# Kernel optimization log

Hardware: AMD Instinct MI355X
Metric: run time of the kernel (lower is better)

## Reference

```python
import jax, jax.numpy as jnp
import numpy as np

U, I, D = 50000, 25000, 128          # users, items, emb_size
E = 1_000_000                        # user-item interactions
L = 3                                # num_layers
B = 4096                             # BPR batch size
N = U + I                            # total graph nodes


def setup_inputs() -> dict:
    key = jax.random.key(0)
    k1, k2, k3, k4, k5, k6, k7 = jax.random.split(key, 7)
    # Xavier-ish embedding tables
    user_emb = jax.random.normal(k1, (U, D), jnp.float32) * 0.1
    item_emb = jax.random.normal(k2, (I, D), jnp.float32) * 0.1
    # random bipartite interactions -> symmetric COO adjacency over N nodes
    eu = jax.random.randint(k3, (E,), 0, U)            # user node ids
    ei = jax.random.randint(k4, (E,), 0, I) + U        # item node ids (offset)
    adj_row = jnp.concatenate([eu, ei]).astype(jnp.int32)   # [2E]
    adj_col = jnp.concatenate([ei, eu]).astype(jnp.int32)   # [2E]
    # symmetric normalization D^-1/2 A D^-1/2 (matches create_adj_mat)
    deg = jax.ops.segment_sum(jnp.ones(2 * E, jnp.float32), adj_row, num_segments=N)
    d_inv = jnp.where(deg > 0, deg ** -0.5, 0.0)
    adj_vals = d_inv[adj_row] * d_inv[adj_col]               # [2E] float32
    users = jax.random.randint(k5, (B,), 0, U).astype(jnp.int32)
    pos_items = jax.random.randint(k6, (B,), 0, I).astype(jnp.int32)
    neg_items = jax.random.randint(k7, (B,), 0, I).astype(jnp.int32)
    return dict(user_emb=user_emb, item_emb=item_emb, adj_row=adj_row,
                adj_col=adj_col, adj_vals=adj_vals, users=users,
                pos_items=pos_items, neg_items=neg_items)


def _spmm(vals, row, col, x):
    # sparse [N,N] @ dense [N,D] via gather + segment_sum
    return jax.ops.segment_sum(vals[:, None] * x[col], row, num_segments=N)


def reference(user_emb, item_emb, adj_row, adj_col, adj_vals,
              users, pos_items, neg_items):
    ego = jnp.concatenate([user_emb, item_emb], axis=0)      # [N, D]
    # FAITHFUL to the torch source: ego_embeddings is never reassigned inside
    # the layer loop, so every one of the L layer outputs equals A @ ego.
    # mean(stack([ego, A@ego, ..., A@ego])) == (ego + L * A@ego) / (L + 1)
    h = _spmm(adj_vals, adj_row, adj_col, ego)               # [N, D]
    final = (ego + L * h) / (L + 1)                          # mean over L+1 layers
    u_final = final[:U]
    i_final = final[U:]
    u_g = u_final[users]                                     # [B, D]
    pos_i_g = i_final[pos_items]                             # [B, D]
    neg_i_g = i_final[neg_items]                             # [B, D]
    return (u_g, pos_i_g, neg_i_g, i_final)
```

## Files before the change

### kernel.cpp

```cpp
#include <hip/hip_runtime.h>
#include <hip/hip_bf16.h>

#define U_CNT 50000
#define I_CNT 25000
#define D_DIM 128
#define E_CNT 1000000
#define B_CNT 4096
#define ICAP 96
#define UCAP 64
#define PNCAP 16
#define BM_WORDS 1600
#define IRANGE (I_CNT / 8)
#define URANGE (U_CNT / 8)
#define NGROUP 1000
#define CHUNK  (E_CNT / NGROUP)
#define BUCKET_BLKS (NGROUP * 8)
#define CVT_BLKS 3125
#define GI_BLKS (8 * 782)
#define GU_BLKS (B_CNT / 4)

typedef int    vi4 __attribute__((ext_vector_type(4)));
typedef float  vf4 __attribute__((ext_vector_type(4)));
typedef float  vf2 __attribute__((ext_vector_type(2)));
typedef unsigned vu4 __attribute__((ext_vector_type(4)));


__device__ __forceinline__ unsigned pack_bf2(float lo, float hi) {
    __hip_bfloat16 a = __float2bfloat16(lo);
    __hip_bfloat16 b = __float2bfloat16(hi);
    unsigned short ua = *reinterpret_cast<unsigned short*>(&a);
    unsigned short ub = *reinterpret_cast<unsigned short*>(&b);
    return ((unsigned)ub << 16) | ua;
}
__device__ __forceinline__ float bf_lo(unsigned w) { return __uint_as_float(w << 16); }
__device__ __forceinline__ float bf_hi(unsigned w) { return __uint_as_float(w & 0xffff0000u); }

__global__ __launch_bounds__(256) void prep_kernel(
        const int* __restrict__ users,
        const int* __restrict__ pos_items,
        const int* __restrict__ neg_items,
        unsigned*  __restrict__ bitmap,
        int*       __restrict__ slot,
        int*       __restrict__ pncnt,
        int*       __restrict__ pnbuck) {
    const int i = blockIdx.x * blockDim.x + threadIdx.x;
    if (i < B_CNT) {
        const int u = users[i];
        atomicOr(&bitmap[u >> 5], 1u << (u & 31));
        atomicCAS(&slot[u], 0, i + 1);
    }
    if (i < 2 * B_CNT) {
        const int idx = (i < B_CNT) ? pos_items[i] : neg_items[i - B_CNT];
        const int c = atomicAdd(&pncnt[idx], 1);
        if (c < PNCAP) pnbuck[idx * PNCAP + c] = B_CNT + i;
    }
}

__global__ __launch_bounds__(256) void bucket_cvt_kernel(
        const int*      __restrict__ adj_row,
        const int*      __restrict__ adj_col,
        const float*    __restrict__ adj_vals,
        const float*    __restrict__ user_emb,
        const unsigned* __restrict__ bitmap,
        const int*      __restrict__ slot,
        int*  __restrict__ icnt,  int*  __restrict__ ucnt,
        int2* __restrict__ ibuck, int2* __restrict__ ubuck,
        unsigned* __restrict__ ue16) {
    if (blockIdx.x < BUCKET_BLKS) {
        const unsigned x = blockIdx.x & 7;
        const int      g = blockIdx.x >> 3;
        const int base = g * CHUNK + (int)threadIdx.x * 4;
        if (base >= g * CHUNK + CHUNK) return;

        const vi4 uu = __builtin_nontemporal_load((const vi4*)(adj_row  + base));
        const vi4 tt = __builtin_nontemporal_load((const vi4*)(adj_col  + base));
        const vf4 vv = __builtin_nontemporal_load((const vf4*)(adj_vals + base));
        const unsigned us[4] = {(unsigned)uu.x, (unsigned)uu.y,
                                (unsigned)uu.z, (unsigned)uu.w};
        const unsigned ts[4] = {(unsigned)(tt.x - U_CNT), (unsigned)(tt.y - U_CNT),
                                (unsigned)(tt.z - U_CNT), (unsigned)(tt.w - U_CNT)};
        const float    vs[4] = {vv.x, vv.y, vv.z, vv.w};
#pragma unroll
        for (int k = 0; k < 4; ++k) {
            const unsigned u = us[k], t = ts[k];
            const int vb = __float_as_int(vs[k]);
            if (t / IRANGE == x) {
                const int c = atomicAdd(&icnt[t], 1);
                ibuck[(size_t)t * ICAP + c] = make_int2((int)u, vb);
            }
            if (u / URANGE == x) {
                if ((bitmap[u >> 5] >> (u & 31)) & 1u) {
                    const int j0 = slot[u] - 1;
                    const int c2 = atomicAdd(&ucnt[j0], 1);
                    ubuck[(size_t)j0 * UCAP + c2] = make_int2((int)t, vb);
                }
            }
        }
    } else {
        const int bid = blockIdx.x - BUCKET_BLKS;
        int i = bid * 1024 + threadIdx.x;
#pragma unroll
        for (int r = 0; r < 4; ++r, i += 256) {
            const vf2 f = __builtin_nontemporal_load(((const vf2*)user_emb) + i);
            __builtin_nontemporal_store(pack_bf2(f.x, f.y), ue16 + i);
        }
    }
}

__global__ __launch_bounds__(256) void gather_kernel(
        const float*    __restrict__ user_emb,
        const float*    __restrict__ item_emb,
        const unsigned* __restrict__ ue16,
        const int*      __restrict__ users,
        const int*      __restrict__ slot,
        const int*      __restrict__ icnt,
        const int*      __restrict__ ucnt,
        const int*      __restrict__ pncnt,
        const int*      __restrict__ pnbuck,
        const int2*     __restrict__ ibuck,
        const int2*     __restrict__ ubuck,
        float*          __restrict__ out) {
    const int lane = threadIdx.x & 63;
    const int wib  = threadIdx.x >> 6;

    if (blockIdx.x < GI_BLKS) {
        const int x  = blockIdx.x & 7;
        const int g  = blockIdx.x >> 3;
        const int li = g * 4 + wib;
        if (li >= IRANGE) return;
        const int t = x * IRANGE + li;

        const int n   = min(icnt[t], ICAP);
        const int2* b = ibuck + (size_t)t * ICAP;
        const int sub = lane >> 4;
        const int cl  = lane & 15;
        float a0=0.f,a1=0.f,a2=0.f,a3=0.f,a4=0.f,a5=0.f,a6=0.f,a7=0.f;

        int q = 0;
        for (; q + 8 <= n; q += 8) {
            const int2 eA = b[q + sub];
            const int2 eB = b[q + 4 + sub];
            const vu4 wA = *(const vu4*)(ue16 + (size_t)eA.x * 64 + cl * 4);
            const vu4 wB = *(const vu4*)(ue16 + (size_t)eB.x * 64 + cl * 4);
            const float vA = __int_as_float(eA.y), vB = __int_as_float(eB.y);
            a0 += vA*bf_lo(wA.x) + vB*bf_lo(wB.x);
            a1 += vA*bf_hi(wA.x) + vB*bf_hi(wB.x);
            a2 += vA*bf_lo(wA.y) + vB*bf_lo(wB.y);
            a3 += vA*bf_hi(wA.y) + vB*bf_hi(wB.y);
            a4 += vA*bf_lo(wA.z) + vB*bf_lo(wB.z);
            a5 += vA*bf_hi(wA.z) + vB*bf_hi(wB.z);
            a6 += vA*bf_lo(wA.w) + vB*bf_lo(wB.w);
            a7 += vA*bf_hi(wA.w) + vB*bf_hi(wB.w);
        }
        if (q + 4 <= n) {
            const int2 e = b[q + sub];
            const vu4 wv = *(const vu4*)(ue16 + (size_t)e.x * 64 + cl * 4);
            const float v = __int_as_float(e.y);
            a0 += v*bf_lo(wv.x); a1 += v*bf_hi(wv.x);
            a2 += v*bf_lo(wv.y); a3 += v*bf_hi(wv.y);
            a4 += v*bf_lo(wv.z); a5 += v*bf_hi(wv.z);
            a6 += v*bf_lo(wv.w); a7 += v*bf_hi(wv.w);
            q += 4;
        }
        if (q < n) {
            const int r = q + sub;
            if (r < n) {
                const int2 e = b[r];
                const vu4 wv = *(const vu4*)(ue16 + (size_t)e.x * 64 + cl * 4);
                const float v = __int_as_float(e.y);
                a0 += v*bf_lo(wv.x); a1 += v*bf_hi(wv.x);
                a2 += v*bf_lo(wv.y); a3 += v*bf_hi(wv.y);
                a4 += v*bf_lo(wv.z); a5 += v*bf_hi(wv.z);
                a6 += v*bf_lo(wv.w); a7 += v*bf_hi(wv.w);
            }
        }
        a0 += __shfl_xor(a0, 16); a0 += __shfl_xor(a0, 32);
        a1 += __shfl_xor(a1, 16); a1 += __shfl_xor(a1, 32);
        a2 += __shfl_xor(a2, 16); a2 += __shfl_xor(a2, 32);
        a3 += __shfl_xor(a3, 16); a3 += __shfl_xor(a3, 32);
        a4 += __shfl_xor(a4, 16); a4 += __shfl_xor(a4, 32);
        a5 += __shfl_xor(a5, 16); a5 += __shfl_xor(a5, 32);
        a6 += __shfl_xor(a6, 16); a6 += __shfl_xor(a6, 32);
        a7 += __shfl_xor(a7, 16); a7 += __shfl_xor(a7, 32);

        if (sub == 0) {
            const float* ie = item_emb + (size_t)t * D_DIM + cl * 8;
            const vf4 g0 = __builtin_nontemporal_load((const vf4*)ie);
            const vf4 g1 = __builtin_nontemporal_load((const vf4*)(ie + 4));
            vf4 o0, o1;
            o0.x = (g0.x + 3.0f*a0)*0.25f; o0.y = (g0.y + 3.0f*a1)*0.25f;
            o0.z = (g0.z + 3.0f*a2)*0.25f; o0.w = (g0.w + 3.0f*a3)*0.25f;
            o1.x = (g1.x + 3.0f*a4)*0.25f; o1.y = (g1.y + 3.0f*a5)*0.25f;
            o1.z = (g1.z + 3.0f*a6)*0.25f; o1.w = (g1.w + 3.0f*a7)*0.25f;
            float* orow = out + (size_t)(3 * B_CNT + t) * D_DIM + cl * 8;
            __builtin_nontemporal_store(o0, (vf4*)orow);
            __builtin_nontemporal_store(o1, (vf4*)(orow + 4));
            const int pn = min(pncnt[t], PNCAP);
            for (int c = 0; c < pn; ++c) {
                const int row = pnbuck[t * PNCAP + c];
                float* pr = out + (size_t)row * D_DIM + cl * 8;
                __builtin_nontemporal_store(o0, (vf4*)pr);
                __builtin_nontemporal_store(o1, (vf4*)(pr + 4));
            }
        }
    } else {
        const int j = (blockIdx.x - GI_BLKS) * 4 + wib;
        const int u  = users[j];
        const int j0 = slot[u] - 1;
        const int n  = min(ucnt[j0], UCAP);
        const int2* b = ubuck + (size_t)j0 * UCAP;
        float ax = 0.0f, ay = 0.0f;
        int q = 0;
        for (; q + 4 <= n; q += 4) {
            const int2 e0 = b[q], e1 = b[q+1], e2 = b[q+2], e3 = b[q+3];
            const float2 x0 = ((const float2*)(item_emb + (size_t)e0.x * D_DIM))[lane];
            const float2 x1 = ((const float2*)(item_emb + (size_t)e1.x * D_DIM))[lane];
            const float2 x2 = ((const float2*)(item_emb + (size_t)e2.x * D_DIM))[lane];
            const float2 x3 = ((const float2*)(item_emb + (size_t)e3.x * D_DIM))[lane];
            const float v0 = __int_as_float(e0.y), v1 = __int_as_float(e1.y);
            const float v2 = __int_as_float(e2.y), v3 = __int_as_float(e3.y);
            ax += v0*x0.x + v1*x1.x + v2*x2.x + v3*x3.x;
            ay += v0*x0.y + v1*x1.y + v2*x2.y + v3*x3.y;
        }
        for (; q < n; ++q) {
            const int2 e = b[q];
            const float2 xx = ((const float2*)(item_emb + (size_t)e.x * D_DIM))[lane];
            const float v = __int_as_float(e.y);
            ax += v * xx.x;
            ay += v * xx.y;
        }
        const float2 eg = ((const float2*)(user_emb + (size_t)u * D_DIM))[lane];
        float2 o;
        o.x = (eg.x + 3.0f * ax) * 0.25f;
        o.y = (eg.y + 3.0f * ay) * 0.25f;
        ((float2*)(out + (size_t)j * D_DIM))[lane] = o;
    }
}

extern "C" void kernel_launch(void* const* d_in, const int* in_sizes, int n_in,
                              void* d_out, int out_size, void* d_ws, size_t ws_size,
                              hipStream_t stream) {
    const float* user_emb  = (const float*)d_in[0];
    const float* item_emb  = (const float*)d_in[1];
    const int*   adj_row   = (const int*)  d_in[2];
    const int*   adj_col   = (const int*)  d_in[3];
    const float* adj_vals  = (const float*)d_in[4];
    const int*   users     = (const int*)  d_in[5];
    const int*   pos_items = (const int*)  d_in[6];
    const int*   neg_items = (const int*)  d_in[7];
    float* out = (float*)d_out;

    unsigned* bitmap = (unsigned*)d_ws;
    int* slot  = (int*)(bitmap + BM_WORDS);
    int* icnt  = slot + U_CNT;
    int* ucnt  = icnt + I_CNT;
    int* pncnt = ucnt + B_CNT;
    int2* ibuck = (int2*)(pncnt + I_CNT);
    int2* ubuck = ibuck + (size_t)I_CNT * ICAP;
    int*  pnbuck = (int*)(ubuck + (size_t)B_CNT * UCAP);
    unsigned* ue16 = (unsigned*)(pnbuck + (size_t)I_CNT * PNCAP);

    const size_t zero_ints = BM_WORDS + U_CNT + I_CNT + B_CNT + I_CNT;
    hipMemsetAsync(bitmap, 0, zero_ints * sizeof(int), stream);

    prep_kernel<<<(2 * B_CNT + 255) / 256, 256, 0, stream>>>(
        users, pos_items, neg_items, bitmap, slot, pncnt, pnbuck);

    bucket_cvt_kernel<<<BUCKET_BLKS + CVT_BLKS, 256, 0, stream>>>(
        adj_row, adj_col, adj_vals, user_emb, bitmap, slot,
        icnt, ucnt, ibuck, ubuck, ue16);

    gather_kernel<<<GI_BLKS + GU_BLKS, 256, 0, stream>>>(
        user_emb, item_emb, ue16, users, slot, icnt, ucnt,
        pncnt, pnbuck, ibuck, ubuck, out);
}
```

Measured before the change: 206.1 us.

## Pack adjacency bucket records into 32 bits and drop slot zeroing

```diff
diff --git a/kernel.cpp b/kernel.cpp
--- a/kernel.cpp
+++ b/kernel.cpp
@@ -1,5 +1,6 @@
 #include <hip/hip_runtime.h>
 #include <hip/hip_bf16.h>
+#include <hip/hip_fp16.h>
 
 #define U_CNT 50000
 #define I_CNT 25000
@@ -19,9 +20,9 @@
 #define GI_BLKS (8 * 782)
 #define GU_BLKS (B_CNT / 4)
 
-typedef int    vi4 __attribute__((ext_vector_type(4)));
-typedef float  vf4 __attribute__((ext_vector_type(4)));
-typedef float  vf2 __attribute__((ext_vector_type(2)));
+typedef int      vi4 __attribute__((ext_vector_type(4)));
+typedef float    vf4 __attribute__((ext_vector_type(4)));
+typedef float    vf2 __attribute__((ext_vector_type(2)));
 typedef unsigned vu4 __attribute__((ext_vector_type(4)));
 
 
@@ -35,19 +36,27 @@
 __device__ __forceinline__ float bf_lo(unsigned w) { return __uint_as_float(w << 16); }
 __device__ __forceinline__ float bf_hi(unsigned w) { return __uint_as_float(w & 0xffff0000u); }
 
+__device__ __forceinline__ unsigned pack_rec(unsigned id, float v) {
+    const __half h = __float2half(v);
+    return id | ((unsigned)__half_as_ushort(h) << 16);
+}
+__device__ __forceinline__ float rec_val(unsigned rec) {
+    return __half2float(__ushort_as_half((unsigned short)(rec >> 16)));
+}
+
 __global__ __launch_bounds__(256) void prep_kernel(
         const int* __restrict__ users,
         const int* __restrict__ pos_items,
         const int* __restrict__ neg_items,
         unsigned*  __restrict__ bitmap,
-        int*       __restrict__ slot,
+        int*       __restrict__ flag,
         int*       __restrict__ pncnt,
         int*       __restrict__ pnbuck) {
     const int i = blockIdx.x * blockDim.x + threadIdx.x;
     if (i < B_CNT) {
         const int u = users[i];
         atomicOr(&bitmap[u >> 5], 1u << (u & 31));
-        atomicCAS(&slot[u], 0, i + 1);
+        flag[u] = i;
     }
     if (i < 2 * B_CNT) {
         const int idx = (i < B_CNT) ? pos_items[i] : neg_items[i - B_CNT];
@@ -62,9 +71,9 @@
         const float*    __restrict__ adj_vals,
         const float*    __restrict__ user_emb,
         const unsigned* __restrict__ bitmap,
-        const int*      __restrict__ slot,
-        int*  __restrict__ icnt,  int*  __restrict__ ucnt,
-        int2* __restrict__ ibuck, int2* __restrict__ ubuck,
+        const int*      __restrict__ flag,
+        int*      __restrict__ icnt,  int*      __restrict__ ucnt,
+        unsigned* __restrict__ ibuck, unsigned* __restrict__ ubuck,
         unsigned* __restrict__ ue16) {
     if (blockIdx.x < BUCKET_BLKS) {
         const unsigned x = blockIdx.x & 7;
@@ -83,16 +92,15 @@
 #pragma unroll
         for (int k = 0; k < 4; ++k) {
             const unsigned u = us[k], t = ts[k];
-            const int vb = __float_as_int(vs[k]);
             if (t / IRANGE == x) {
                 const int c = atomicAdd(&icnt[t], 1);
-                ibuck[(size_t)t * ICAP + c] = make_int2((int)u, vb);
+                ibuck[(size_t)t * ICAP + c] = pack_rec(u, vs[k]);
             }
             if (u / URANGE == x) {
                 if ((bitmap[u >> 5] >> (u & 31)) & 1u) {
-                    const int j0 = slot[u] - 1;
+                    const int j0 = flag[u];
                     const int c2 = atomicAdd(&ucnt[j0], 1);
-                    ubuck[(size_t)j0 * UCAP + c2] = make_int2((int)t, vb);
+                    ubuck[(size_t)j0 * UCAP + c2] = pack_rec(t, vs[k]);
                 }
             }
         }
@@ -112,13 +120,13 @@
         const float*    __restrict__ item_emb,
         const unsigned* __restrict__ ue16,
         const int*      __restrict__ users,
-        const int*      __restrict__ slot,
+        const int*      __restrict__ flag,
         const int*      __restrict__ icnt,
         const int*      __restrict__ ucnt,
         const int*      __restrict__ pncnt,
         const int*      __restrict__ pnbuck,
-        const int2*     __restrict__ ibuck,
-        const int2*     __restrict__ ubuck,
+        const unsigned* __restrict__ ibuck,
+        const unsigned* __restrict__ ubuck,
         float*          __restrict__ out) {
     const int lane = threadIdx.x & 63;
     const int wib  = threadIdx.x >> 6;
@@ -130,19 +138,19 @@
         if (li >= IRANGE) return;
         const int t = x * IRANGE + li;
 
-        const int n   = min(icnt[t], ICAP);
-        const int2* b = ibuck + (size_t)t * ICAP;
+        const int n = min(icnt[t], ICAP);
+        const unsigned* b = ibuck + (size_t)t * ICAP;
         const int sub = lane >> 4;
         const int cl  = lane & 15;
         float a0=0.f,a1=0.f,a2=0.f,a3=0.f,a4=0.f,a5=0.f,a6=0.f,a7=0.f;
 
         int q = 0;
         for (; q + 8 <= n; q += 8) {
-            const int2 eA = b[q + sub];
-            const int2 eB = b[q + 4 + sub];
-            const vu4 wA = *(const vu4*)(ue16 + (size_t)eA.x * 64 + cl * 4);
-            const vu4 wB = *(const vu4*)(ue16 + (size_t)eB.x * 64 + cl * 4);
-            const float vA = __int_as_float(eA.y), vB = __int_as_float(eB.y);
+            const unsigned eA = b[q + sub];
+            const unsigned eB = b[q + 4 + sub];
+            const vu4 wA = *(const vu4*)(ue16 + (size_t)(eA & 0xFFFFu) * 64 + cl * 4);
+            const vu4 wB = *(const vu4*)(ue16 + (size_t)(eB & 0xFFFFu) * 64 + cl * 4);
+            const float vA = rec_val(eA), vB = rec_val(eB);
             a0 += vA*bf_lo(wA.x) + vB*bf_lo(wB.x);
             a1 += vA*bf_hi(wA.x) + vB*bf_hi(wB.x);
             a2 += vA*bf_lo(wA.y) + vB*bf_lo(wB.y);
@@ -153,9 +161,9 @@
             a7 += vA*bf_hi(wA.w) + vB*bf_hi(wB.w);
         }
         if (q + 4 <= n) {
-            const int2 e = b[q + sub];
-            const vu4 wv = *(const vu4*)(ue16 + (size_t)e.x * 64 + cl * 4);
-            const float v = __int_as_float(e.y);
+            const unsigned e = b[q + sub];
+            const vu4 wv = *(const vu4*)(ue16 + (size_t)(e & 0xFFFFu) * 64 + cl * 4);
+            const float v = rec_val(e);
             a0 += v*bf_lo(wv.x); a1 += v*bf_hi(wv.x);
             a2 += v*bf_lo(wv.y); a3 += v*bf_hi(wv.y);
             a4 += v*bf_lo(wv.z); a5 += v*bf_hi(wv.z);
@@ -165,9 +173,9 @@
         if (q < n) {
             const int r = q + sub;
             if (r < n) {
-                const int2 e = b[r];
-                const vu4 wv = *(const vu4*)(ue16 + (size_t)e.x * 64 + cl * 4);
-                const float v = __int_as_float(e.y);
+                const unsigned e = b[r];
+                const vu4 wv = *(const vu4*)(ue16 + (size_t)(e & 0xFFFFu) * 64 + cl * 4);
+                const float v = rec_val(e);
                 a0 += v*bf_lo(wv.x); a1 += v*bf_hi(wv.x);
                 a2 += v*bf_lo(wv.y); a3 += v*bf_hi(wv.y);
                 a4 += v*bf_lo(wv.z); a5 += v*bf_hi(wv.z);
@@ -206,26 +214,26 @@
     } else {
         const int j = (blockIdx.x - GI_BLKS) * 4 + wib;
         const int u  = users[j];
-        const int j0 = slot[u] - 1;
+        const int j0 = flag[u];
         const int n  = min(ucnt[j0], UCAP);
-        const int2* b = ubuck + (size_t)j0 * UCAP;
+        const unsigned* b = ubuck + (size_t)j0 * UCAP;
         float ax = 0.0f, ay = 0.0f;
         int q = 0;
         for (; q + 4 <= n; q += 4) {
-            const int2 e0 = b[q], e1 = b[q+1], e2 = b[q+2], e3 = b[q+3];
-            const float2 x0 = ((const float2*)(item_emb + (size_t)e0.x * D_DIM))[lane];
-            const float2 x1 = ((const float2*)(item_emb + (size_t)e1.x * D_DIM))[lane];
-            const float2 x2 = ((const float2*)(item_emb + (size_t)e2.x * D_DIM))[lane];
-            const float2 x3 = ((const float2*)(item_emb + (size_t)e3.x * D_DIM))[lane];
-            const float v0 = __int_as_float(e0.y), v1 = __int_as_float(e1.y);
-            const float v2 = __int_as_float(e2.y), v3 = __int_as_float(e3.y);
+            const unsigned e0 = b[q], e1 = b[q+1], e2 = b[q+2], e3 = b[q+3];
+            const float2 x0 = ((const float2*)(item_emb + (size_t)(e0 & 0xFFFFu) * D_DIM))[lane];
+            const float2 x1 = ((const float2*)(item_emb + (size_t)(e1 & 0xFFFFu) * D_DIM))[lane];
+            const float2 x2 = ((const float2*)(item_emb + (size_t)(e2 & 0xFFFFu) * D_DIM))[lane];
+            const float2 x3 = ((const float2*)(item_emb + (size_t)(e3 & 0xFFFFu) * D_DIM))[lane];
+            const float v0 = rec_val(e0), v1 = rec_val(e1);
+            const float v2 = rec_val(e2), v3 = rec_val(e3);
             ax += v0*x0.x + v1*x1.x + v2*x2.x + v3*x3.x;
             ay += v0*x0.y + v1*x1.y + v2*x2.y + v3*x3.y;
         }
         for (; q < n; ++q) {
-            const int2 e = b[q];
-            const float2 xx = ((const float2*)(item_emb + (size_t)e.x * D_DIM))[lane];
-            const float v = __int_as_float(e.y);
+            const unsigned e = b[q];
+            const float2 xx = ((const float2*)(item_emb + (size_t)(e & 0xFFFFu) * D_DIM))[lane];
+            const float v = rec_val(e);
             ax += v * xx.x;
             ay += v * xx.y;
         }
@@ -251,26 +259,26 @@
     float* out = (float*)d_out;
 
     unsigned* bitmap = (unsigned*)d_ws;
-    int* slot  = (int*)(bitmap + BM_WORDS);
-    int* icnt  = slot + U_CNT;
+    int* icnt  = (int*)(bitmap + BM_WORDS);
     int* ucnt  = icnt + I_CNT;
     int* pncnt = ucnt + B_CNT;
-    int2* ibuck = (int2*)(pncnt + I_CNT);
-    int2* ubuck = ibuck + (size_t)I_CNT * ICAP;
-    int*  pnbuck = (int*)(ubuck + (size_t)B_CNT * UCAP);
-    unsigned* ue16 = (unsigned*)(pnbuck + (size_t)I_CNT * PNCAP);
-
-    const size_t zero_ints = BM_WORDS + U_CNT + I_CNT + B_CNT + I_CNT;
+    int* flag  = pncnt + I_CNT;
+    int* pnbuck = flag + U_CNT;
+    unsigned* ibuck = (unsigned*)(pnbuck + (size_t)I_CNT * PNCAP);
+    unsigned* ubuck = ibuck + (size_t)I_CNT * ICAP;
+    unsigned* ue16  = ubuck + (size_t)B_CNT * UCAP;
+
+    const size_t zero_ints = BM_WORDS + I_CNT + B_CNT + I_CNT;
     hipMemsetAsync(bitmap, 0, zero_ints * sizeof(int), stream);
 
     prep_kernel<<<(2 * B_CNT + 255) / 256, 256, 0, stream>>>(
-        users, pos_items, neg_items, bitmap, slot, pncnt, pnbuck);
+        users, pos_items, neg_items, bitmap, flag, pncnt, pnbuck);
 
     bucket_cvt_kernel<<<BUCKET_BLKS + CVT_BLKS, 256, 0, stream>>>(
-        adj_row, adj_col, adj_vals, user_emb, bitmap, slot,
+        adj_row, adj_col, adj_vals, user_emb, bitmap, flag,
         icnt, ucnt, ibuck, ubuck, ue16);
 
     gather_kernel<<<GI_BLKS + GU_BLKS, 256, 0, stream>>>(
-        user_emb, item_emb, ue16, users, slot, icnt, ucnt,
+        user_emb, item_emb, ue16, users, flag, icnt, ucnt,
         pncnt, pnbuck, ibuck, ubuck, out);
 }
```

New measurement: 204.6 us. Within noise of the previous version (-0.8%).
